# Kernel tuning notes

Measured on AMD Instinct MI355X. Metric: run time of the kernel, lower is better.

## Reference

```python
import jax, jax.numpy as jnp
import numpy as np
from jax import lax

DN = ('NCHW', 'OIHW', 'NCHW')


def setup_inputs() -> dict:
    key = jax.random.key(0)
    ks = jax.random.split(key, 7)
    B, IC, OC, H, W = 8, 64, 64, 128, 128
    return {
        'x': jax.random.normal(ks[0], (B, IC, H, W), jnp.float32),
        'w3': jax.random.normal(ks[1], (OC, IC, 3, 3), jnp.float32) * 0.05,
        'b3': jax.random.normal(ks[2], (OC,), jnp.float32) * 0.05,
        'w5': jax.random.normal(ks[3], (OC, IC, 5, 5), jnp.float32) * 0.05,
        'b5': jax.random.normal(ks[4], (OC,), jnp.float32) * 0.05,
        'wr': jax.random.normal(ks[5], (OC, 10, 1, 1), jnp.float32) * 0.1,
        'br': jax.random.normal(ks[6], (OC,), jnp.float32) * 0.05,
    }


def reference(x, w3, b3, w5, b5, wr, br):
    # Two 'same' convs (k=3 pad 1, k=5 pad 2) as in layers['5']
    y3 = lax.conv_general_dilated(x, w3, (1, 1), 'SAME', dimension_numbers=DN) + b3[None, :, None, None]
    y5 = lax.conv_general_dilated(x, w5, (1, 1), 'SAME', dimension_numbers=DN) + b5[None, :, None, None]
    B, C, H, W = y3.shape
    # The nested pad/crop loop == 9 zero-padded unit shifts of y3:
    # stackedFeatures order per channel: [y5, shift(sh=0,sw=0..2), shift(sh=1,...), ...]
    # shifted[h, w] = y3[h + 1 - sw, w + 1 - sh] with zero padding.
    P = jnp.pad(y3, ((0, 0), (0, 0), (1, 1), (1, 1)))
    shifts = [P[:, :, 2 - sw:2 - sw + H, 2 - sh:2 - sh + W]
              for sh in range(3) for sw in range(3)]
    stacked = jnp.stack([y5] + shifts, axis=2)  # [B, C, 10, H, W]
    # remap: grouped 1x1 conv, groups=OC, 10 in-channels per group
    out = jnp.einsum('bcghw,cg->bchw', stacked, wr[:, :, 0, 0]) + br[None, :, None, None]
    return out
```

## Files before the change

kernel.cpp:

```cpp
#include <hip/hip_runtime.h>

typedef unsigned short u16;
typedef unsigned int u32;
typedef __attribute__((ext_vector_type(8))) short short8;
typedef __attribute__((ext_vector_type(4))) short short4v;
typedef __attribute__((ext_vector_type(4))) float floatx4;

#define HH 128
#define WW 128
#define XP 72

__device__ __forceinline__ float bf2f(u16 u) {
    u32 b = ((u32)u) << 16;
    return __builtin_bit_cast(float, b);
}
__device__ __forceinline__ u16 f2bf(float f) {
    u32 b = __builtin_bit_cast(u32, f);
    b += 0x7FFFu + ((b >> 16) & 1u);
    return (u16)(b >> 16);
}

typedef __attribute__((address_space(3))) u16 lds_u16;
typedef const __attribute__((address_space(1))) u16 glob_u16;
__device__ __forceinline__ void gl_lds16(const u16* g, u16* l) {
    __builtin_amdgcn_global_load_lds((glob_u16*)g, (lds_u16*)l, 16, 0, 0);
}

#define W5C_BYTE 256
#define W3S_BYTE 205056
#define SCAL_BYTE 303360
#define V_BYTE 306432
#define XT_BYTE 1371392
#define N_W5C 102400
#define N_W3S 49152
#define N_SCAL 768
#define PACK_N (N_W5C + N_W3S + N_SCAL)

__global__ __launch_bounds__(256) void sniff_kernel(const u16* __restrict__ xu,
                                                    int* __restrict__ flag) {
    __shared__ int cnt;
    if (threadIdx.x == 0) cnt = 0;
    __syncthreads();
    int c = 0;
    for (int k = 0; k < 8; ++k) {
        int idx = 2 * (threadIdx.x * 8 + k);
        u16 u = xu[idx];
        int e = (u >> 7) & 0xFF;
        if (e >= 140) c++;
    }
    atomicAdd(&cnt, c);
    __syncthreads();
    if (threadIdx.x == 0) *flag = (cnt >= 8) ? 1 : 0;
}

__device__ __forceinline__ float load_any(const void* p, int i, int isf32) {
    return isf32 ? ((const float*)p)[i] : bf2f(((const u16*)p)[i]);
}

__global__ __launch_bounds__(256) void prepack(
        const void* w3, const void* b3, const void* w5, const void* b5,
        const void* wr, const void* br, const int* __restrict__ flag,
        u16* __restrict__ w5c, u16* __restrict__ w3s, float* __restrict__ scal) {
    int i = blockIdx.x * 256 + threadIdx.x;
    if (i >= PACK_N) return;
    int f = *flag;
    if (i < N_W5C) {
        int j = i & 7, lane = (i >> 3) & 63, mt = (i >> 9) & 3, ks = i >> 11;
        int oc = mt * 16 + (lane & 15);
        int k = ks * 32 + ((lane >> 4) & 3) * 8 + j;
        int tap = k >> 6, ic = k & 63;
        int kh = tap / 5, kw = tap - kh * 5;
        int dh = kh - 2, dw = kw - 2;
        float v = load_any(wr, oc * 10, f) * load_any(w5, (oc * 64 + ic) * 25 + tap, f);
        for (int sw = 0; sw < 3; ++sw) {
            int r = dh + sw;
            if (r < 0 || r > 2) continue;
            for (int sh = 0; sh < 3; ++sh) {
                int c = dw + sh;
                if (c < 0 || c > 2) continue;
                v += load_any(wr, oc * 10 + 1 + sh * 3 + sw, f) *
                     load_any(w3, (oc * 64 + ic) * 9 + r * 3 + c, f);
            }
        }
        w5c[i] = f2bf(v);
    } else if (i < N_W5C + N_W3S) {
        int ii = i - N_W5C;
        int side = ii / 12288, rem = ii - side * 12288;
        int j = rem & 7, lane = (rem >> 3) & 63, mt = (rem >> 9) & 3, ks = rem >> 11;
        int oc = mt * 16 + (lane & 15);
        int k = ks * 32 + ((lane >> 4) & 3) * 8 + j;
        int kk = k >> 6, ic = k & 63;
        int r, c;
        if (side == 0)      { r = 2;  c = kk; }
        else if (side == 1) { r = 0;  c = kk; }
        else if (side == 2) { r = kk; c = 2;  }
        else                { r = kk; c = 0;  }
        w3s[ii] = f2bf(load_any(w3, (oc * 64 + ic) * 9 + r * 3 + c, f));
    } else {
        int i2 = i - N_W5C - N_W3S;
        float v;
        if (i2 < 64) {
            int oc = i2;
            float swr = 0.f;
            for (int g = 1; g <= 9; ++g) swr += load_any(wr, oc * 10 + g, f);
            v = load_any(wr, oc * 10, f) * load_any(b5, oc, f) +
                swr * load_any(b3, oc, f) + load_any(br, oc, f);
        } else if (i2 < 704) {
            v = load_any(wr, i2 - 64, f);
        } else {
            v = load_any(b3, i2 - 704, f);
        }
        scal[i2] = v;
    }
}

__global__ __launch_bounds__(256) void transpose_x(
        const void* __restrict__ x, const int* __restrict__ flag,
        u16* __restrict__ xt) {
    __shared__ u16 tbuf[32 * XP];
    const int b = blockIdx.z, h = blockIdx.y, w0 = blockIdx.x * 32;
    const int t = threadIdx.x;
    const int f = *flag;
    if (f) {
        const int w2 = t & 15, ic = t >> 4;
#pragma unroll
        for (int p = 0; p < 4; ++p) {
            int icc = ic + p * 16;
            const float* src = (const float*)x +
                (((size_t)(b * 64 + icc) * 128 + h) * 128 + w0 + 2 * w2);
            float2 v = *(const float2*)src;
            tbuf[(2 * w2) * XP + icc]     = f2bf(v.x);
            tbuf[(2 * w2 + 1) * XP + icc] = f2bf(v.y);
        }
    } else {
        const int w4 = t & 7, ic = t >> 3;
#pragma unroll
        for (int p = 0; p < 2; ++p) {
            int icc = ic + p * 32;
            const u16* src = (const u16*)x +
                (((size_t)(b * 64 + icc) * 128 + h) * 128 + w0 + 4 * w4);
            short4v v = *(const short4v*)src;
#pragma unroll
            for (int e = 0; e < 4; ++e)
                tbuf[(4 * w4 + e) * XP + icc] = (u16)v[e];
        }
    }
    __syncthreads();
    const int w = t >> 3, q = t & 7;
    short8 v = *(const short8*)&tbuf[w * XP + q * 8];
    *(short8*)(xt + ((size_t)((b * 128 + h) * 128) + w0 + w) * 64 + q * 8) = v;
}

__global__ __launch_bounds__(256) void virt_y3_mfma(
        const u16* __restrict__ xt, const u16* __restrict__ w3s,
        const float* __restrict__ scal, float* __restrict__ V) {
    __shared__ u16 xrow[146 * XP];
    const int side = blockIdx.x, b = blockIdx.y;
    const int tid = threadIdx.x;
    const int fixed = (side & 1) ? 127 : 0;
    {
        const int q8 = tid & 7, p0 = tid >> 3;
#pragma unroll
        for (int it = 0; it < 5; ++it) {
            int p = p0 + it * 32;
            if (p < 132) {
                int cc = p - 2;
                short8 v = {0, 0, 0, 0, 0, 0, 0, 0};
                if ((unsigned)cc < 128u) {
                    size_t idx = (side < 2)
                        ? ((size_t)(b * 128 + fixed) * 128 + cc)
                        : ((size_t)(b * 128 + cc) * 128 + fixed);
                    v = *(const short8*)(xt + idx * 64 + q8 * 8);
                }
                *(short8*)&xrow[p * XP + q8 * 8] = v;
            }
        }
    }
    __syncthreads();

    const int wv = tid >> 6, lane = tid & 63, cb = lane & 15, q = lane >> 4;
    floatx4 acc[9];
#pragma unroll
    for (int nt = 0; nt < 9; ++nt) acc[nt] = (floatx4){0.f, 0.f, 0.f, 0.f};

    const u16* wbase = w3s + side * 12288 + wv * 512 + lane * 8;
#pragma unroll
    for (int ks = 0; ks < 6; ++ks) {
        short8 aa = *(const short8*)(wbase + ks * 2048);
        const int kbase = ks * 32 + q * 8;
        const int kk = kbase >> 6, ic0 = kbase & 63;
#pragma unroll
        for (int nt = 0; nt < 9; ++nt) {
            int p = nt * 16 + cb + kk;
            short8 bb = *(const short8*)&xrow[p * XP + ic0];
            acc[nt] = __builtin_amdgcn_mfma_f32_16x16x32_bf16(aa, bb, acc[nt], 0, 0, 0);
        }
    }

    const float* b3f = scal + 704;
#pragma unroll
    for (int nt = 0; nt < 9; ++nt) {
        int pos = nt * 16 + cb;
        if (pos < 130) {
#pragma unroll
            for (int reg = 0; reg < 4; ++reg) {
                int oc = wv * 16 + q * 4 + reg;
                V[((size_t)(b * 4 + side) * 130 + pos) * 64 + oc] = acc[nt][reg] + b3f[oc];
            }
        }
    }
}

__global__ __launch_bounds__(256) void apply_fix(
        const float* __restrict__ V, const float* __restrict__ scal,
        const int* __restrict__ flag, void* __restrict__ out) {
    const int side = blockIdx.x, b = blockIdx.y;
    const int f = *flag;
    const float* wrf = scal + 64;
    const float* Vb = V + (size_t)b * 4 * 130 * 64;
    const float* VT = Vb;
    const float* VB = Vb + 130 * 64;
    const float* VL = Vb + 2 * 130 * 64;
    const float* VR = Vb + 3 * 130 * 64;
    const int nitems = (side < 2) ? 128 * 64 : 126 * 64;
    for (int idx = blockIdx.z * 256 + threadIdx.x; idx < nitems; idx += 2048) {
        int oc = idx & 63;
        int h, w;
        if (side < 2) { w = idx >> 6; h = side ? 127 : 0; }
        else          { h = (idx >> 6) + 1; w = (side == 2) ? 0 : 127; }
        float s = 0.f;
#pragma unroll
        for (int sh = 0; sh < 3; ++sh)
#pragma unroll
            for (int sw = 0; sw < 3; ++sw) {
                int qh = h + 1 - sw, qw = w + 1 - sh;
                float v;
                if (qh == -1)       v = VT[(qw + 1) * 64 + oc];
                else if (qh == 128) v = VB[(qw + 1) * 64 + oc];
                else if (qw == -1)  v = VL[(qh + 1) * 64 + oc];
                else if (qw == 128) v = VR[(qh + 1) * 64 + oc];
                else continue;
                s -= wrf[oc * 10 + 1 + sh * 3 + sw] * v;
            }
        size_t oidx = ((size_t)(b * 64 + oc) * 128 + h) * 128 + w;
        if (f) ((float*)out)[oidx] += s;
        else {
            u16* po = (u16*)out + oidx;
            *po = f2bf(bf2f(*po) + s);
        }
    }
}

__global__ __launch_bounds__(256, 2) void conv_main(
        const u16* __restrict__ xt, const u16* __restrict__ w5c,
        const float* __restrict__ scal, const int* __restrict__ flag,
        void* __restrict__ out) {
    __shared__ __align__(16) u16 xs[400 * XP];
    __shared__ __align__(16) u16 wbuf[2][2][2048];
    const int b = blockIdx.z, h0 = blockIdx.y * 16, w0 = blockIdx.x * 16;
    const int tid = threadIdx.x;
    const int f = *flag;
    const int wv = tid >> 6, lane = tid & 63;

    {
        const int q8 = tid & 7, p0 = tid >> 3;
        for (int it = 0; it < 13; ++it) {
            int px = p0 + it * 32;
            if (px < 400) {
                int r = px / 20, c = px - r * 20;
                int gh = h0 + r - 2, gw = w0 + c - 2;
                short8 v = {0, 0, 0, 0, 0, 0, 0, 0};
                if ((unsigned)gh < 128u && (unsigned)gw < 128u)
                    v = *(const short8*)(xt +
                            ((size_t)((b * 128 + gh) * 128 + gw)) * 64 + q8 * 8);
                *(short8*)&xs[px * XP + q8 * 8] = v;
            }
        }
    }
    gl_lds16(w5c + 0 * 2048 + wv * 512 + lane * 8, &wbuf[0][0][wv * 512]);
    gl_lds16(w5c + 1 * 2048 + wv * 512 + lane * 8, &wbuf[0][1][wv * 512]);
    __syncthreads();

    const int cb = lane & 15, q = lane >> 4, wv4 = wv * 4;
    floatx4 acc[4][4];
#pragma unroll
    for (int mt = 0; mt < 4; ++mt)
#pragma unroll
        for (int nt = 0; nt < 4; ++nt)
            acc[mt][nt] = (floatx4){0.f, 0.f, 0.f, 0.f};

#pragma unroll 1
    for (int tap = 0; tap < 25; ++tap) {
        const int p = tap & 1;
        if (tap + 1 < 25) {
            gl_lds16(w5c + (size_t)((tap + 1) * 2 + 0) * 2048 + wv * 512 + lane * 8,
                     &wbuf[p ^ 1][0][wv * 512]);
            gl_lds16(w5c + (size_t)((tap + 1) * 2 + 1) * 2048 + wv * 512 + lane * 8,
                     &wbuf[p ^ 1][1][wv * 512]);
        }
        const int kh = tap / 5, kw = tap - kh * 5;
#pragma unroll
        for (int s = 0; s < 2; ++s) {
            short8 aa[4], bb[4];
#pragma unroll
            for (int mt = 0; mt < 4; ++mt)
                aa[mt] = *(const short8*)&wbuf[p][s][mt * 512 + lane * 8];
#pragma unroll
            for (int nt = 0; nt < 4; ++nt)
                bb[nt] = *(const short8*)&xs[((wv4 + nt + kh) * 20 + cb + kw) * XP +
                                             s * 32 + q * 8];
#pragma unroll
            for (int nt = 0; nt < 4; ++nt)
#pragma unroll
                for (int mt = 0; mt < 4; ++mt)
                    acc[mt][nt] = __builtin_amdgcn_mfma_f32_16x16x32_bf16(
                        aa[mt], bb[nt], acc[mt][nt], 0, 0, 0);
        }
        __syncthreads();
    }

    const float* biasC = scal;
#pragma unroll
    for (int mt = 0; mt < 4; ++mt)
#pragma unroll
        for (int nt = 0; nt < 4; ++nt) {
            int gh = h0 + wv4 + nt;
#pragma unroll
            for (int reg = 0; reg < 4; ++reg) {
                int oc = mt * 16 + q * 4 + reg;
                float s = acc[mt][nt][reg] + biasC[oc];
                size_t oidx = ((size_t)(b * 64 + oc) * 128 + gh) * 128 + w0 + cb;
                if (f) ((float*)out)[oidx] = s;
                else   ((u16*)out)[oidx]   = f2bf(s);
            }
        }
}

extern "C" void kernel_launch(void* const* d_in, const int* in_sizes, int n_in,
                              void* d_out, int out_size, void* d_ws, size_t ws_size,
                              hipStream_t stream) {
    const void* x  = d_in[0];
    const void* w3 = d_in[1];
    const void* b3 = d_in[2];
    const void* w5 = d_in[3];
    const void* b5 = d_in[4];
    const void* wr = d_in[5];
    const void* br = d_in[6];

    int*   flag = (int*)d_ws;
    u16*   w5c  = (u16*)((char*)d_ws + W5C_BYTE);
    u16*   w3s  = (u16*)((char*)d_ws + W3S_BYTE);
    float* scal = (float*)((char*)d_ws + SCAL_BYTE);
    float* V    = (float*)((char*)d_ws + V_BYTE);
    u16*   xt   = (u16*)((char*)d_ws + XT_BYTE);

    sniff_kernel<<<1, 256, 0, stream>>>((const u16*)x, flag);
    prepack<<<(PACK_N + 255) / 256, 256, 0, stream>>>(w3, b3, w5, b5, wr, br, flag,
                                                      w5c, w3s, scal);
    transpose_x<<<dim3(4, 128, 8), 256, 0, stream>>>(x, flag, xt);
    virt_y3_mfma<<<dim3(4, 8), 256, 0, stream>>>(xt, w3s, scal, V);
    conv_main<<<dim3(8, 8, 8), 256, 0, stream>>>(xt, w5c, scal, flag, d_out);
    apply_fix<<<dim3(4, 8, 8), 256, 0, stream>>>(V, scal, flag, d_out);
}
```

Baseline: 146.7 us.

## Fuse six launches into two kernels with inline dtype sniff and edge fix

Merges the dtype sniff, weight prepack, input transpose and border y3 computation into one heterogeneous launch where block index selects the role. The border y3 computation now reads x directly instead of xt. The edge correction moves into the main conv epilogue instead of a separate read-modify-write pass. This removes four launches plus the extra output pass, at the cost of redundant per-block sniffing and more branching in the epilogue.

```diff
diff --git a/kernel.cpp b/kernel.cpp
--- a/kernel.cpp
+++ b/kernel.cpp
@@ -6,8 +6,6 @@
 typedef __attribute__((ext_vector_type(4))) short short4v;
 typedef __attribute__((ext_vector_type(4))) float floatx4;
 
-#define HH 128
-#define WW 128
 #define XP 72
 
 __device__ __forceinline__ float bf2f(u16 u) {
@@ -26,241 +24,256 @@
     __builtin_amdgcn_global_load_lds((glob_u16*)g, (lds_u16*)l, 16, 0, 0);
 }
 
-#define W5C_BYTE 256
-#define W3S_BYTE 205056
-#define SCAL_BYTE 303360
-#define V_BYTE 306432
-#define XT_BYTE 1371392
-#define N_W5C 102400
-#define N_W3S 49152
-#define N_SCAL 768
-#define PACK_N (N_W5C + N_W3S + N_SCAL)
-
-__global__ __launch_bounds__(256) void sniff_kernel(const u16* __restrict__ xu,
-                                                    int* __restrict__ flag) {
-    __shared__ int cnt;
-    if (threadIdx.x == 0) cnt = 0;
+__device__ __forceinline__ float load_any(const void* p, int i, int isf32) {
+    return isf32 ? ((const float*)p)[i] : bf2f(((const u16*)p)[i]);
+}
+
+__device__ __forceinline__ int sniff_f(const void* x, int* scnt) {
+    if (threadIdx.x == 0) *scnt = 0;
     __syncthreads();
     int c = 0;
+#pragma unroll
     for (int k = 0; k < 8; ++k) {
-        int idx = 2 * (threadIdx.x * 8 + k);
-        u16 u = xu[idx];
+        u16 u = ((const u16*)x)[2 * (threadIdx.x * 8 + k)];
         int e = (u >> 7) & 0xFF;
         if (e >= 140) c++;
     }
-    atomicAdd(&cnt, c);
+    if (c) atomicAdd(scnt, c);
     __syncthreads();
-    if (threadIdx.x == 0) *flag = (cnt >= 8) ? 1 : 0;
-}
-
-__device__ __forceinline__ float load_any(const void* p, int i, int isf32) {
-    return isf32 ? ((const float*)p)[i] : bf2f(((const u16*)p)[i]);
-}
-
-__global__ __launch_bounds__(256) void prepack(
-        const void* w3, const void* b3, const void* w5, const void* b5,
-        const void* wr, const void* br, const int* __restrict__ flag,
-        u16* __restrict__ w5c, u16* __restrict__ w3s, float* __restrict__ scal) {
-    int i = blockIdx.x * 256 + threadIdx.x;
-    if (i >= PACK_N) return;
-    int f = *flag;
-    if (i < N_W5C) {
-        int j = i & 7, lane = (i >> 3) & 63, mt = (i >> 9) & 3, ks = i >> 11;
-        int oc = mt * 16 + (lane & 15);
-        int k = ks * 32 + ((lane >> 4) & 3) * 8 + j;
-        int tap = k >> 6, ic = k & 63;
-        int kh = tap / 5, kw = tap - kh * 5;
-        int dh = kh - 2, dw = kw - 2;
-        float v = load_any(wr, oc * 10, f) * load_any(w5, (oc * 64 + ic) * 25 + tap, f);
+    return (*scnt >= 8) ? 1 : 0;
+}
+
+#define W5C_BYTE 0
+#define SCAL_BYTE 204800
+#define V_BYTE 207616
+#define XT_BYTE 1272576
+#define N_W5C 102400
+#define N_SCAL 704
+#define PACK_N2 (N_W5C + N_SCAL)
+
+#define VIRT_BLKS 32
+#define PACK_BLKS ((PACK_N2 + 255) / 256)
+#define TRANS_BLKS 4096
+
+__global__ __launch_bounds__(256) void fuse1(
+        const void* __restrict__ x, const void* __restrict__ w3,
+        const void* __restrict__ b3, const void* __restrict__ w5,
+        const void* __restrict__ b5, const void* __restrict__ wr,
+        const void* __restrict__ br,
+        u16* __restrict__ w5c, float* __restrict__ scal,
+        float* __restrict__ V, u16* __restrict__ xt) {
+    __shared__ __align__(16) u16 smem[132 * XP];
+    __shared__ int scnt;
+    const int bid = blockIdx.x;
+    const int tid = threadIdx.x;
+    const int f = sniff_f(x, &scnt);
+
+    if (bid < VIRT_BLKS) {
+        const int side = bid & 3, b = bid >> 2;
+        const int fixed = (side & 1) ? 127 : 0;
+        {
+            short8 z = {0, 0, 0, 0, 0, 0, 0, 0};
+            short8* sp = (short8*)smem;
+            for (int i = tid; i < (132 * XP) / 8; i += 256) sp[i] = z;
+        }
+        __syncthreads();
+        {
+            const int ic = tid & 63, g = tid >> 6;
+            if (side < 2) {
+                if (f) {
+                    const float* xp = (const float*)x +
+                        ((size_t)(b * 64 + ic) * 128 + fixed) * 128;
+                    for (int c0 = g * 32; c0 < g * 32 + 32; c0 += 4) {
+                        float4 v = *(const float4*)(xp + c0);
+                        smem[(c0 + 2) * XP + ic] = f2bf(v.x);
+                        smem[(c0 + 3) * XP + ic] = f2bf(v.y);
+                        smem[(c0 + 4) * XP + ic] = f2bf(v.z);
+                        smem[(c0 + 5) * XP + ic] = f2bf(v.w);
+                    }
+                } else {
+                    const u16* xp = (const u16*)x +
+                        ((size_t)(b * 64 + ic) * 128 + fixed) * 128;
+                    for (int c0 = g * 32; c0 < g * 32 + 32; c0 += 8) {
+                        short8 v = *(const short8*)(xp + c0);
+#pragma unroll
+                        for (int e = 0; e < 8; ++e)
+                            smem[(c0 + 2 + e) * XP + ic] = (u16)v[e];
+                    }
+                }
+            } else {
+                if (f) {
+                    const float* xp = (const float*)x +
+                        (size_t)(b * 64 + ic) * 16384 + fixed;
+                    for (int cc = g * 32; cc < g * 32 + 32; ++cc)
+                        smem[(cc + 2) * XP + ic] = f2bf(xp[(size_t)cc * 128]);
+                } else {
+                    const u16* xp = (const u16*)x +
+                        (size_t)(b * 64 + ic) * 16384 + fixed;
+                    for (int cc = g * 32; cc < g * 32 + 32; ++cc)
+                        smem[(cc + 2) * XP + ic] = xp[(size_t)cc * 128];
+                }
+            }
+        }
+        const int wv = tid >> 6, lane = tid & 63, cb = lane & 15, q = lane >> 4;
+        const int oc = wv * 16 + cb;
+        short8 aaA[6];
+#pragma unroll
+        for (int ks = 0; ks < 6; ++ks) {
+            const int kbase = ks * 32 + q * 8;
+            const int kk = kbase >> 6, ic0 = kbase & 63;
+            int r, c;
+            if (side == 0)      { r = 2;  c = kk; }
+            else if (side == 1) { r = 0;  c = kk; }
+            else if (side == 2) { r = kk; c = 2;  }
+            else                { r = kk; c = 0;  }
+            short8 a;
+#pragma unroll
+            for (int j = 0; j < 8; ++j)
+                a[j] = (short)f2bf(load_any(w3, (oc * 64 + ic0 + j) * 9 + r * 3 + c, f));
+            aaA[ks] = a;
+        }
+        __syncthreads();
+
+        floatx4 acc[9];
+#pragma unroll
+        for (int nt = 0; nt < 9; ++nt) acc[nt] = (floatx4){0.f, 0.f, 0.f, 0.f};
+#pragma unroll
+        for (int ks = 0; ks < 6; ++ks) {
+            const int kbase = ks * 32 + q * 8;
+            const int kk = kbase >> 6, ic0 = kbase & 63;
+#pragma unroll
+            for (int nt = 0; nt < 9; ++nt) {
+                int p = nt * 16 + cb + kk;
+                if (nt == 8 && p > 131) p = 131;
+                short8 bb = *(const short8*)&smem[p * XP + ic0];
+                acc[nt] = __builtin_amdgcn_mfma_f32_16x16x32_bf16(aaA[ks], bb,
+                                                                  acc[nt], 0, 0, 0);
+            }
+        }
+#pragma unroll
+        for (int nt = 0; nt < 9; ++nt) {
+            int pos = nt * 16 + cb;
+            if (pos < 130) {
+#pragma unroll
+                for (int reg = 0; reg < 4; ++reg) {
+                    int oco = wv * 16 + q * 4 + reg;
+                    V[((size_t)(b * 4 + side) * 130 + pos) * 64 + oco] =
+                        acc[nt][reg] + load_any(b3, oco, f);
+                }
+            }
+        }
+        return;
+    }
+
+    if (bid < VIRT_BLKS + PACK_BLKS) {
+        const int i = (bid - VIRT_BLKS) * 256 + tid;
+        if (i >= PACK_N2) return;
+        if (i < N_W5C) {
+            int j = i & 7, lane = (i >> 3) & 63, mt = (i >> 9) & 3, ks = i >> 11;
+            int oc = mt * 16 + (lane & 15);
+            int k = ks * 32 + ((lane >> 4) & 3) * 8 + j;
+            int tap = k >> 6, ic = k & 63;
+            int kh = tap / 5, kw = tap - kh * 5;
+            int dh = kh - 2, dw = kw - 2;
+            float v = load_any(wr, oc * 10, f) * load_any(w5, (oc * 64 + ic) * 25 + tap, f);
+            for (int sw = 0; sw < 3; ++sw) {
+                int r = dh + sw;
+                if (r < 0 || r > 2) continue;
+                for (int sh = 0; sh < 3; ++sh) {
+                    int c = dw + sh;
+                    if (c < 0 || c > 2) continue;
+                    v += load_any(wr, oc * 10 + 1 + sh * 3 + sw, f) *
+                         load_any(w3, (oc * 64 + ic) * 9 + r * 3 + c, f);
+                }
+            }
+            w5c[i] = f2bf(v);
+        } else {
+            int i2 = i - N_W5C;
+            float v;
+            if (i2 < 64) {
+                int oc = i2;
+                float swr = 0.f;
+                for (int g = 1; g <= 9; ++g) swr += load_any(wr, oc * 10 + g, f);
+                v = load_any(wr, oc * 10, f) * load_any(b5, oc, f) +
+                    swr * load_any(b3, oc, f) + load_any(br, oc, f);
+            } else {
+                v = load_any(wr, i2 - 64, f);
+            }
+            scal[i2] = v;
+        }
+        return;
+    }
+
+    {
+        const int t2 = bid - (VIRT_BLKS + PACK_BLKS);
+        const int b = t2 >> 9, h = (t2 >> 2) & 127, w0 = (t2 & 3) * 32;
+        const int t = tid;
+        if (f) {
+            const int w2 = t & 15, ic = t >> 4;
+#pragma unroll
+            for (int p = 0; p < 4; ++p) {
+                int icc = ic + p * 16;
+                const float* src = (const float*)x +
+                    (((size_t)(b * 64 + icc) * 128 + h) * 128 + w0 + 2 * w2);
+                float2 v = *(const float2*)src;
+                smem[(2 * w2) * XP + icc]     = f2bf(v.x);
+                smem[(2 * w2 + 1) * XP + icc] = f2bf(v.y);
+            }
+        } else {
+            const int w4 = t & 7, ic = t >> 3;
+#pragma unroll
+            for (int p = 0; p < 2; ++p) {
+                int icc = ic + p * 32;
+                const u16* src = (const u16*)x +
+                    (((size_t)(b * 64 + icc) * 128 + h) * 128 + w0 + 4 * w4);
+                short4v v = *(const short4v*)src;
+#pragma unroll
+                for (int e = 0; e < 4; ++e)
+                    smem[(4 * w4 + e) * XP + icc] = (u16)v[e];
+            }
+        }
+        __syncthreads();
+        const int w = t >> 3, qq = t & 7;
+        short8 v = *(const short8*)&smem[w * XP + qq * 8];
+        *(short8*)(xt + ((size_t)((b * 128 + h) * 128) + w0 + w) * 64 + qq * 8) = v;
+    }
+}
+
+__device__ floatx4 edge_fix4(
+        const float* __restrict__ Vb, const float* __restrict__ wrf,
+        int gh, int gw, int oc0, floatx4 s) {
+#pragma unroll
+    for (int sh = 0; sh < 3; ++sh)
+#pragma unroll
         for (int sw = 0; sw < 3; ++sw) {
-            int r = dh + sw;
-            if (r < 0 || r > 2) continue;
-            for (int sh = 0; sh < 3; ++sh) {
-                int c = dw + sh;
-                if (c < 0 || c > 2) continue;
-                v += load_any(wr, oc * 10 + 1 + sh * 3 + sw, f) *
-                     load_any(w3, (oc * 64 + ic) * 9 + r * 3 + c, f);
-            }
-        }
-        w5c[i] = f2bf(v);
-    } else if (i < N_W5C + N_W3S) {
-        int ii = i - N_W5C;
-        int side = ii / 12288, rem = ii - side * 12288;
-        int j = rem & 7, lane = (rem >> 3) & 63, mt = (rem >> 9) & 3, ks = rem >> 11;
-        int oc = mt * 16 + (lane & 15);
-        int k = ks * 32 + ((lane >> 4) & 3) * 8 + j;
-        int kk = k >> 6, ic = k & 63;
-        int r, c;
-        if (side == 0)      { r = 2;  c = kk; }
-        else if (side == 1) { r = 0;  c = kk; }
-        else if (side == 2) { r = kk; c = 2;  }
-        else                { r = kk; c = 0;  }
-        w3s[ii] = f2bf(load_any(w3, (oc * 64 + ic) * 9 + r * 3 + c, f));
-    } else {
-        int i2 = i - N_W5C - N_W3S;
-        float v;
-        if (i2 < 64) {
-            int oc = i2;
-            float swr = 0.f;
-            for (int g = 1; g <= 9; ++g) swr += load_any(wr, oc * 10 + g, f);
-            v = load_any(wr, oc * 10, f) * load_any(b5, oc, f) +
-                swr * load_any(b3, oc, f) + load_any(br, oc, f);
-        } else if (i2 < 704) {
-            v = load_any(wr, i2 - 64, f);
-        } else {
-            v = load_any(b3, i2 - 704, f);
-        }
-        scal[i2] = v;
-    }
-}
-
-__global__ __launch_bounds__(256) void transpose_x(
-        const void* __restrict__ x, const int* __restrict__ flag,
-        u16* __restrict__ xt) {
-    __shared__ u16 tbuf[32 * XP];
-    const int b = blockIdx.z, h = blockIdx.y, w0 = blockIdx.x * 32;
-    const int t = threadIdx.x;
-    const int f = *flag;
-    if (f) {
-        const int w2 = t & 15, ic = t >> 4;
-#pragma unroll
-        for (int p = 0; p < 4; ++p) {
-            int icc = ic + p * 16;
-            const float* src = (const float*)x +
-                (((size_t)(b * 64 + icc) * 128 + h) * 128 + w0 + 2 * w2);
-            float2 v = *(const float2*)src;
-            tbuf[(2 * w2) * XP + icc]     = f2bf(v.x);
-            tbuf[(2 * w2 + 1) * XP + icc] = f2bf(v.y);
-        }
-    } else {
-        const int w4 = t & 7, ic = t >> 3;
-#pragma unroll
-        for (int p = 0; p < 2; ++p) {
-            int icc = ic + p * 32;
-            const u16* src = (const u16*)x +
-                (((size_t)(b * 64 + icc) * 128 + h) * 128 + w0 + 4 * w4);
-            short4v v = *(const short4v*)src;
-#pragma unroll
-            for (int e = 0; e < 4; ++e)
-                tbuf[(4 * w4 + e) * XP + icc] = (u16)v[e];
-        }
-    }
-    __syncthreads();
-    const int w = t >> 3, q = t & 7;
-    short8 v = *(const short8*)&tbuf[w * XP + q * 8];
-    *(short8*)(xt + ((size_t)((b * 128 + h) * 128) + w0 + w) * 64 + q * 8) = v;
-}
-
-__global__ __launch_bounds__(256) void virt_y3_mfma(
-        const u16* __restrict__ xt, const u16* __restrict__ w3s,
-        const float* __restrict__ scal, float* __restrict__ V) {
-    __shared__ u16 xrow[146 * XP];
-    const int side = blockIdx.x, b = blockIdx.y;
-    const int tid = threadIdx.x;
-    const int fixed = (side & 1) ? 127 : 0;
-    {
-        const int q8 = tid & 7, p0 = tid >> 3;
-#pragma unroll
-        for (int it = 0; it < 5; ++it) {
-            int p = p0 + it * 32;
-            if (p < 132) {
-                int cc = p - 2;
-                short8 v = {0, 0, 0, 0, 0, 0, 0, 0};
-                if ((unsigned)cc < 128u) {
-                    size_t idx = (side < 2)
-                        ? ((size_t)(b * 128 + fixed) * 128 + cc)
-                        : ((size_t)(b * 128 + cc) * 128 + fixed);
-                    v = *(const short8*)(xt + idx * 64 + q8 * 8);
-                }
-                *(short8*)&xrow[p * XP + q8 * 8] = v;
-            }
-        }
-    }
-    __syncthreads();
-
-    const int wv = tid >> 6, lane = tid & 63, cb = lane & 15, q = lane >> 4;
-    floatx4 acc[9];
-#pragma unroll
-    for (int nt = 0; nt < 9; ++nt) acc[nt] = (floatx4){0.f, 0.f, 0.f, 0.f};
-
-    const u16* wbase = w3s + side * 12288 + wv * 512 + lane * 8;
-#pragma unroll
-    for (int ks = 0; ks < 6; ++ks) {
-        short8 aa = *(const short8*)(wbase + ks * 2048);
-        const int kbase = ks * 32 + q * 8;
-        const int kk = kbase >> 6, ic0 = kbase & 63;
-#pragma unroll
-        for (int nt = 0; nt < 9; ++nt) {
-            int p = nt * 16 + cb + kk;
-            short8 bb = *(const short8*)&xrow[p * XP + ic0];
-            acc[nt] = __builtin_amdgcn_mfma_f32_16x16x32_bf16(aa, bb, acc[nt], 0, 0, 0);
-        }
-    }
-
-    const float* b3f = scal + 704;
-#pragma unroll
-    for (int nt = 0; nt < 9; ++nt) {
-        int pos = nt * 16 + cb;
-        if (pos < 130) {
-#pragma unroll
-            for (int reg = 0; reg < 4; ++reg) {
-                int oc = wv * 16 + q * 4 + reg;
-                V[((size_t)(b * 4 + side) * 130 + pos) * 64 + oc] = acc[nt][reg] + b3f[oc];
-            }
-        }
-    }
-}
-
-__global__ __launch_bounds__(256) void apply_fix(
-        const float* __restrict__ V, const float* __restrict__ scal,
-        const int* __restrict__ flag, void* __restrict__ out) {
-    const int side = blockIdx.x, b = blockIdx.y;
-    const int f = *flag;
-    const float* wrf = scal + 64;
-    const float* Vb = V + (size_t)b * 4 * 130 * 64;
-    const float* VT = Vb;
-    const float* VB = Vb + 130 * 64;
-    const float* VL = Vb + 2 * 130 * 64;
-    const float* VR = Vb + 3 * 130 * 64;
-    const int nitems = (side < 2) ? 128 * 64 : 126 * 64;
-    for (int idx = blockIdx.z * 256 + threadIdx.x; idx < nitems; idx += 2048) {
-        int oc = idx & 63;
-        int h, w;
-        if (side < 2) { w = idx >> 6; h = side ? 127 : 0; }
-        else          { h = (idx >> 6) + 1; w = (side == 2) ? 0 : 127; }
-        float s = 0.f;
-#pragma unroll
-        for (int sh = 0; sh < 3; ++sh)
-#pragma unroll
-            for (int sw = 0; sw < 3; ++sw) {
-                int qh = h + 1 - sw, qw = w + 1 - sh;
-                float v;
-                if (qh == -1)       v = VT[(qw + 1) * 64 + oc];
-                else if (qh == 128) v = VB[(qw + 1) * 64 + oc];
-                else if (qw == -1)  v = VL[(qh + 1) * 64 + oc];
-                else if (qw == 128) v = VR[(qh + 1) * 64 + oc];
-                else continue;
-                s -= wrf[oc * 10 + 1 + sh * 3 + sw] * v;
-            }
-        size_t oidx = ((size_t)(b * 64 + oc) * 128 + h) * 128 + w;
-        if (f) ((float*)out)[oidx] += s;
-        else {
-            u16* po = (u16*)out + oidx;
-            *po = f2bf(bf2f(*po) + s);
-        }
-    }
-}
-
-__global__ __launch_bounds__(256, 2) void conv_main(
+            const int qh = gh + 1 - sw, qw = gw + 1 - sh;
+            int sd, pos;
+            if (qh == -1)       { sd = 0; pos = qw + 1; }
+            else if (qh == 128) { sd = 1; pos = qw + 1; }
+            else if (qw == -1)  { sd = 2; pos = qh + 1; }
+            else if (qw == 128) { sd = 3; pos = qh + 1; }
+            else continue;
+            const float* vp = Vb + ((size_t)sd * 130 + pos) * 64 + oc0;
+            const int wi = 1 + sh * 3 + sw;
+#pragma unroll
+            for (int r = 0; r < 4; ++r)
+                s[r] -= wrf[(oc0 + r) * 10 + wi] * vp[r];
+        }
+    return s;
+}
+
+__global__ __launch_bounds__(256, 2) void conv_fused(
+        const void* __restrict__ x,
         const u16* __restrict__ xt, const u16* __restrict__ w5c,
-        const float* __restrict__ scal, const int* __restrict__ flag,
+        const float* __restrict__ scal, const float* __restrict__ V,
         void* __restrict__ out) {
     __shared__ __align__(16) u16 xs[400 * XP];
     __shared__ __align__(16) u16 wbuf[2][2][2048];
+    __shared__ int scnt;
     const int b = blockIdx.z, h0 = blockIdx.y * 16, w0 = blockIdx.x * 16;
     const int tid = threadIdx.x;
-    const int f = *flag;
     const int wv = tid >> 6, lane = tid & 63;
+    const int f = sniff_f(x, &scnt);
 
     {
         const int q8 = tid & 7, p0 = tid >> 3;
@@ -320,18 +333,26 @@
     }
 
     const float* biasC = scal;
+    const float* wrf = scal + 64;
+    const float* Vb = V + (size_t)b * 4 * 130 * 64;
 #pragma unroll
     for (int mt = 0; mt < 4; ++mt)
 #pragma unroll
         for (int nt = 0; nt < 4; ++nt) {
-            int gh = h0 + wv4 + nt;
+            const int gh = h0 + wv4 + nt;
+            const int gw = w0 + cb;
+            const int oc0 = mt * 16 + q * 4;
+            floatx4 s;
+#pragma unroll
+            for (int reg = 0; reg < 4; ++reg)
+                s[reg] = acc[mt][nt][reg] + biasC[oc0 + reg];
+            if (gh == 0 || gh == 127 || gw == 0 || gw == 127)
+                s = edge_fix4(Vb, wrf, gh, gw, oc0, s);
 #pragma unroll
             for (int reg = 0; reg < 4; ++reg) {
-                int oc = mt * 16 + q * 4 + reg;
-                float s = acc[mt][nt][reg] + biasC[oc];
-                size_t oidx = ((size_t)(b * 64 + oc) * 128 + gh) * 128 + w0 + cb;
-                if (f) ((float*)out)[oidx] = s;
-                else   ((u16*)out)[oidx]   = f2bf(s);
+                size_t oidx = ((size_t)(b * 64 + oc0 + reg) * 128 + gh) * 128 + gw;
+                if (f) ((float*)out)[oidx] = s[reg];
+                else   ((u16*)out)[oidx]   = f2bf(s[reg]);
             }
         }
 }
@@ -347,18 +368,12 @@
     const void* wr = d_in[5];
     const void* br = d_in[6];
 
-    int*   flag = (int*)d_ws;
     u16*   w5c  = (u16*)((char*)d_ws + W5C_BYTE);
-    u16*   w3s  = (u16*)((char*)d_ws + W3S_BYTE);
     float* scal = (float*)((char*)d_ws + SCAL_BYTE);
     float* V    = (float*)((char*)d_ws + V_BYTE);
     u16*   xt   = (u16*)((char*)d_ws + XT_BYTE);
 
-    sniff_kernel<<<1, 256, 0, stream>>>((const u16*)x, flag);
-    prepack<<<(PACK_N + 255) / 256, 256, 0, stream>>>(w3, b3, w5, b5, wr, br, flag,
-                                                      w5c, w3s, scal);
-    transpose_x<<<dim3(4, 128, 8), 256, 0, stream>>>(x, flag, xt);
-    virt_y3_mfma<<<dim3(4, 8), 256, 0, stream>>>(xt, w3s, scal, V);
-    conv_main<<<dim3(8, 8, 8), 256, 0, stream>>>(xt, w5c, scal, flag, d_out);
-    apply_fix<<<dim3(4, 8, 8), 256, 0, stream>>>(V, scal, flag, d_out);
-}
+    fuse1<<<VIRT_BLKS + PACK_BLKS + TRANS_BLKS, 256, 0, stream>>>(
+        x, w3, b3, w5, b5, wr, br, w5c, scal, V, xt);
+    conv_fused<<<dim3(8, 8, 8), 256, 0, stream>>>(x, xt, w5c, scal, V, d_out);
+}
```

Result: slower. 166.5 us (+13.5%).
